# Kernel optimization log

Measured on AMD Instinct MI355X. Metric: run time of the kernel, lower is better.

## Reference

```python
import jax, jax.numpy as jnp
import numpy as np

B, NQ, NA = 2, 4096, 2048
DIM_INP, DIM, HID, NBLK, K = 512, 512, 512, 5, 8


def _pe(p):
    # NeRF positional encoding, L=10: [sin(f0*p), cos(f0*p), sin(f1*p), ...] -> 60 dims
    freqs = (2.0 ** jnp.arange(10, dtype=p.dtype)) * jnp.pi
    a = p[..., None, :] * freqs[:, None]          # [..., 10, 3]
    out = jnp.stack([jnp.sin(a), jnp.cos(a)], axis=-2)  # [..., 10, 2, 3]
    return out.reshape(*p.shape[:-1], 60)


def _forward(xyz_q, global_feats, anchors_xyz, anchors_feats,
             w_qs, w_ks, w_vs, w_kg, w_vg,
             d1_w, d1_b, d2_w, d2_b, g1_w, g1_b, g2_w, g2_b,
             fc_p_w, fc_p_b, fc_c_w, fc_c_b, blk0_w, blk0_b, blk1_w, blk1_b):
    # ---- KNN (torch.no_grad equivalent) ----
    q = jax.lax.stop_gradient(xyz_q)
    a = jax.lax.stop_gradient(anchors_xyz)
    d2 = (jnp.sum(q * q, -1)[:, :, None] + jnp.sum(a * a, -1)[:, None, :]
          - 2.0 * jnp.einsum('bqd,bnd->bqn', q, a))        # [B,NQ,NA]
    _, knn_idx = jax.lax.top_k(-d2, K)                      # [B,NQ,K] smallest dists

    gather = jax.vmap(lambda t, i: t[i])                    # per-batch gather

    # ---- cross-transformer (vector attention over K local + 1 global token) ----
    q_attn = global_feats @ w_qs                            # [B,DIM]
    kg = jnp.broadcast_to((global_feats @ w_kg)[:, None, None, :], (B, NQ, 1, DIM))
    vg = jnp.broadcast_to((global_feats @ w_vg)[:, None, None, :], (B, NQ, 1, DIM))
    k_attn = jnp.concatenate([gather(anchors_feats @ w_ks, knn_idx), kg], axis=2)  # [B,NQ,K+1,DIM]
    v_attn = jnp.concatenate([gather(anchors_feats @ w_vs, knn_idx), vg], axis=2)

    xyz_k = gather(anchors_xyz, knn_idx)                    # [B,NQ,K,3]
    d = xyz_q[:, :, None] - xyz_k                           # relative positions
    pe_loc = jax.nn.relu(d @ d1_w + d1_b) @ d2_w + d2_b     # fc_delta, [B,NQ,K,DIM]
    pos = jnp.concatenate([pe_loc, jnp.zeros((B, NQ, 1, DIM), pe_loc.dtype)], axis=2)

    attn_in = q_attn[:, None, None, :] - k_attn + pos
    attn = jax.nn.relu(attn_in @ g1_w + g1_b) @ g2_w + g2_b # fc_gamma
    attn = jax.nn.softmax(attn, axis=-2)                    # softmax over neighbor axis
    lat = jnp.einsum('bmnf,bmnf->bmf', attn, v_attn + pos)  # [B,NQ,DIM]

    # ---- occupancy decoder ----
    net = _pe(xyz_q) @ fc_p_w + fc_p_b                      # [B,NQ,HID]
    for i in range(NBLK):
        net = net + lat @ fc_c_w[i] + fc_c_b[i]
        h = jax.nn.relu(net) @ blk0_w[i] + blk0_b[i]
        net = net + (jax.nn.relu(h) @ blk1_w[i] + blk1_b[i])  # ResnetBlockFC (shortcut=identity)
    return net


def setup_inputs() -> dict:
    key = jax.random.key(0)
    ks = jax.random.split(key, 32)
    r = lambda i, shape, s=0.02: jax.random.normal(ks[i], shape, jnp.float32) * s
    return {
        'xyz_q': jax.random.uniform(ks[0], (B, NQ, 3), jnp.float32),
        'global_feats': jax.random.normal(ks[2], (B, DIM_INP), jnp.float32),
        'anchors_xyz': jax.random.uniform(ks[1], (B, NA, 3), jnp.float32),
        'anchors_feats': jax.random.normal(ks[3], (B, NA, DIM_INP), jnp.float32),
        'w_qs': r(4, (DIM_INP, DIM)), 'w_ks': r(5, (DIM_INP, DIM)), 'w_vs': r(6, (DIM_INP, DIM)),
        'w_kg': r(7, (DIM_INP, DIM)), 'w_vg': r(8, (DIM_INP, DIM)),
        'd1_w': r(9, (3, DIM)), 'd1_b': r(10, (DIM,)),
        'd2_w': r(11, (DIM, DIM)), 'd2_b': r(12, (DIM,)),
        'g1_w': r(13, (DIM, DIM)), 'g1_b': r(14, (DIM,)),
        'g2_w': r(15, (DIM, DIM)), 'g2_b': r(16, (DIM,)),
        'fc_p_w': r(17, (60, HID)), 'fc_p_b': r(18, (HID,)),
        'fc_c_w': r(19, (NBLK, DIM, HID)), 'fc_c_b': r(20, (NBLK, HID)),
        'blk0_w': r(21, (NBLK, HID, HID)), 'blk0_b': r(22, (NBLK, HID)),
        'blk1_w': r(23, (NBLK, HID, HID)), 'blk1_b': r(24, (NBLK, HID)),
    }


def reference(xyz_q, global_feats, anchors_xyz, anchors_feats,
              w_qs, w_ks, w_vs, w_kg, w_vg,
              d1_w, d1_b, d2_w, d2_b, g1_w, g1_b, g2_w, g2_b,
              fc_p_w, fc_p_b, fc_c_w, fc_c_b, blk0_w, blk0_b, blk1_w, blk1_b):
    return _forward(xyz_q, global_feats, anchors_xyz, anchors_feats,
                    w_qs, w_ks, w_vs, w_kg, w_vg,
                    d1_w, d1_b, d2_w, d2_b, g1_w, g1_b, g2_w, g2_b,
                    fc_p_w, fc_p_b, fc_c_w, fc_c_b, blk0_w, blk0_b, blk1_w, blk1_b)
```

## Files before the change

### kernel.cpp

```cpp
#include <hip/hip_runtime.h>

#define B 2
#define NQ 4096
#define NA 2048
#define CH 1024
#define LDK 40

typedef __attribute__((ext_vector_type(8))) short bf16x8;
typedef __attribute__((ext_vector_type(4))) float f32x4;

__device__ __forceinline__ float b2f(unsigned short u){ union{unsigned i; float f;} c; c.i=((unsigned)u)<<16; return c.f; }
__device__ __forceinline__ unsigned short f2b(float f){ union{float f; unsigned u;} c; c.f=f; unsigned u=c.u; u += 0x7FFFu + ((u>>16)&1u); return (unsigned short)(u>>16); }
__device__ __forceinline__ void split2(float x, short& h, short& l){
    unsigned short hh = f2b(x); h = (short)hh; l = (short)f2b(x - b2f(hh));
}
__device__ __forceinline__ float4 ld4(const float* p){ return *(const float4*)p; }

__device__ __forceinline__ void gld_lds16(const void* g, void* s) {
    __builtin_amdgcn_global_load_lds(
        (__attribute__((address_space(1))) unsigned int*)g,
        (__attribute__((address_space(3))) unsigned int*)s,
        16, 0, 0);
}

__global__ __launch_bounds__(256) void proj_small(
    const float* __restrict__ gf,
    const float* __restrict__ w_qs, const float* __restrict__ w_kg, const float* __restrict__ w_vg,
    float* __restrict__ q_attn, float* __restrict__ kgv, float* __restrict__ vgv)
{
    int mat = blockIdx.x >> 1, b = blockIdx.x & 1;
    const float* W = (mat==0) ? w_qs : (mat==1 ? w_kg : w_vg);
    float* O       = (mat==0) ? q_attn : (mat==1 ? kgv : vgv);
    __shared__ float sg[512];
    int t = threadIdx.x;
    for (int i=t;i<512;i+=256) sg[i] = gf[b*512+i];
    __syncthreads();
    for (int c=t;c<512;c+=256) {
        float acc = 0.f;
        for (int k=0;k<512;k++) acc = fmaf(sg[k], W[k*512+c], acc);
        O[b*512+c] = acc;
    }
}

__global__ __launch_bounds__(256) void knn_kernel(
    const float* __restrict__ xyz_q, const float* __restrict__ axyz, int* __restrict__ knn)
{
    __shared__ float sax[NA], say[NA], saz[NA];
    const int t = threadIdx.x;
    const int b  = blockIdx.x >> 9;
    const int qi = t >> 5;
    const int q  = ((blockIdx.x & 511) << 3) + qi;
    const int g  = t & 31;
    for (int i=t;i<NA;i+=256) {
        const float* ap = axyz + (size_t)(b*NA+i)*3;
        sax[i]=ap[0]; say[i]=ap[1]; saz[i]=ap[2];
    }
    __syncthreads();
    const double qx = (double)xyz_q[(size_t)(b*NQ+q)*3+0];
    const double qy = (double)xyz_q[(size_t)(b*NQ+q)*3+1];
    const double qz = (double)xyz_q[(size_t)(b*NQ+q)*3+2];
    const double qq = (qx*qx + qy*qy) + qz*qz;
    double best[8]; int bid[8];
    #pragma unroll
    for (int j=0;j<8;j++){ best[j]=1.0e300; bid[j]=0; }
    for (int jj=0; jj<64; jj++) {
        const int i = jj*32 + g;
        double ax=(double)sax[i], ay=(double)say[i], az=(double)saz[i];
        double aa  = (ax*ax + ay*ay) + az*az;
        double dot = (qx*ax + qy*ay) + qz*az;
        double dd  = (qq + aa) - 2.0*dot;
        if (dd < best[7]) {
            best[7]=dd; bid[7]=i;
            #pragma unroll
            for (int j=7;j>0;--j) if (best[j] < best[j-1]) {
                double tf=best[j]; best[j]=best[j-1]; best[j-1]=tf;
                int ti=bid[j]; bid[j]=bid[j-1]; bid[j-1]=ti;
            }
        }
    }
    #pragma unroll
    for (int s=16; s>=1; s>>=1) {
        double pb[8]; int pbi[8];
        #pragma unroll
        for (int j=0;j<8;j++){
            pb[j]  = __shfl_xor(best[j], s, 64);
            pbi[j] = __shfl_xor(bid[j],  s, 64);
        }
        #pragma unroll
        for (int i=0;i<8;i++) {
            double bo = pb[7-i]; int boi = pbi[7-i];
            if (bo < best[i]) { best[i]=bo; bid[i]=boi; }
        }
        #pragma unroll
        for (int i=0;i<4;i++) {
            if (best[i] > best[i+4]) {
                double td=best[i]; best[i]=best[i+4]; best[i+4]=td;
                int ti=bid[i]; bid[i]=bid[i+4]; bid[i+4]=ti;
            }
        }
        #pragma unroll
        for (int ii=0;ii<2;ii++)
        #pragma unroll
        for (int jj2=0;jj2<2;jj2++) {
            int i = ii*4 + jj2;
            if (best[i] > best[i+2]) {
                double td=best[i]; best[i]=best[i+2]; best[i+2]=td;
                int ti=bid[i]; bid[i]=bid[i+2]; bid[i+2]=ti;
            }
        }
        #pragma unroll
        for (int ii=0;ii<4;ii++) {
            int i = ii*2;
            if (best[i] > best[i+1]) {
                double td=best[i]; best[i]=best[i+1]; best[i+1]=td;
                int ti=bid[i]; bid[i]=bid[i+1]; bid[i+1]=ti;
            }
        }
    }
    if (g == 0) {
        #pragma unroll
        for (int j=0;j<8;j++) knn[(size_t)(b*NQ+q)*8+j] = bid[j];
    }
}

__global__ __launch_bounds__(256) void prep_w5(
    const float* __restrict__ W0, const float* __restrict__ W1, const float* __restrict__ W2,
    const float* __restrict__ W3, const float* __restrict__ W4,
    short* __restrict__ O0, short* __restrict__ O1, short* __restrict__ O2,
    short* __restrict__ O3, short* __restrict__ O4)
{
    const int m = blockIdx.x >> 7;
    const float* W = (m==0)?W0:(m==1)?W1:(m==2)?W2:(m==3)?W3:W4;
    short* Wb      = (m==0)?O0:(m==1)?O1:(m==2)?O2:(m==3)?O3:O4;
    const int gid = (blockIdx.x & 127)*256 + threadIdx.x;
    const int n  = gid & 511;
    const int kc = (gid >> 9) * 8;
    short o[8];
    #pragma unroll
    for (int j=0;j<8;j++) o[j] = (short)f2b(W[(size_t)(kc+j)*512 + n]);
    *(short4*)&Wb[(size_t)n*512 + kc]     = make_short4(o[0],o[1],o[2],o[3]);
    *(short4*)&Wb[(size_t)n*512 + kc + 4] = make_short4(o[4],o[5],o[6],o[7]);
}
__global__ __launch_bounds__(256) void prep_w3(
    const float* __restrict__ W0, const float* __restrict__ W1, const float* __restrict__ W2,
    short* __restrict__ H0, short* __restrict__ L0,
    short* __restrict__ H1, short* __restrict__ L1,
    short* __restrict__ H2, short* __restrict__ L2)
{
    const int m = blockIdx.x >> 7;
    const float* W = (m==0)?W0:(m==1)?W1:W2;
    short* Wh = (m==0)?H0:(m==1)?H1:H2;
    short* Wl = (m==0)?L0:(m==1)?L1:L2;
    const int gid = (blockIdx.x & 127)*256 + threadIdx.x;
    const int n  = gid & 511;
    const int kc = (gid >> 9) * 8;
    short hi[8], lo[8];
    #pragma unroll
    for (int j=0;j<8;j++) split2(W[(size_t)(kc+j)*512 + n], hi[j], lo[j]);
    *(short4*)&Wh[(size_t)n*512 + kc]     = make_short4(hi[0],hi[1],hi[2],hi[3]);
    *(short4*)&Wh[(size_t)n*512 + kc + 4] = make_short4(hi[4],hi[5],hi[6],hi[7]);
    *(short4*)&Wl[(size_t)n*512 + kc]     = make_short4(lo[0],lo[1],lo[2],lo[3]);
    *(short4*)&Wl[(size_t)n*512 + kc + 4] = make_short4(lo[4],lo[5],lo[6],lo[7]);
}

__global__ __launch_bounds__(256) void cvt_bf16(
    const float* __restrict__ X, short* __restrict__ Xb)
{
    const size_t i0 = ((size_t)blockIdx.x*256 + threadIdx.x)*8;
    float4 a = *(const float4*)(X+i0), bq = *(const float4*)(X+i0+4);
    float v[8] = {a.x,a.y,a.z,a.w,bq.x,bq.y,bq.z,bq.w};
    short o[8];
    #pragma unroll
    for (int j=0;j<8;j++) o[j] = (short)f2b(v[j]);
    *(short4*)(Xb+i0)   = make_short4(o[0],o[1],o[2],o[3]);
    *(short4*)(Xb+i0+4) = make_short4(o[4],o[5],o[6],o[7]);
}

template<int OUT_MODE, int RELU_OUT>
__global__ __launch_bounds__(256) void gemm1(
    const short* __restrict__ Ab, const short* __restrict__ Wb,
    const float* __restrict__ bias,
    float* __restrict__ Cf, short* __restrict__ Cb)
{
    __shared__ short As[64*LDK], Bs[64*LDK];
    const int t = threadIdx.x;
    const int row0 = blockIdx.y*64, col0 = blockIdx.x*64;
    const int lane = t & 63, w = t >> 6;
    const int m0 = (w>>1)*32, n0 = (w&1)*32;
    const int fl = lane & 15, quad = lane >> 4;
    const int s_row = t >> 2, s_k = (t & 3) * 8;

    f32x4 zero = {0.f,0.f,0.f,0.f};
    f32x4 acc[2][2];
    acc[0][0]=zero; acc[0][1]=zero; acc[1][0]=zero; acc[1][1]=zero;

    const size_t a_base = (size_t)(row0+s_row)*512 + s_k;
    const size_t b_base = (size_t)(col0+s_row)*512 + s_k;
    int4 ra = *(const int4*)(Ab + a_base);
    int4 rb = *(const int4*)(Wb + b_base);

    for (int k0 = 0; k0 < 512; k0 += 32) {
        *(int4*)&As[s_row*LDK + s_k] = ra;
        *(int4*)&Bs[s_row*LDK + s_k] = rb;
        __syncthreads();
        if (k0 + 32 < 512) {
            ra = *(const int4*)(Ab + a_base + k0 + 32);
            rb = *(const int4*)(Wb + b_base + k0 + 32);
        }
        bf16x8 fa[2], fb[2];
        #pragma unroll
        for (int i=0;i<2;i++) {
            fa[i] = *(const bf16x8*)&As[(m0 + i*16 + fl)*LDK + quad*8];
            fb[i] = *(const bf16x8*)&Bs[(n0 + i*16 + fl)*LDK + quad*8];
        }
        #pragma unroll
        for (int i=0;i<2;i++)
        #pragma unroll
        for (int j=0;j<2;j++)
            acc[i][j] = __builtin_amdgcn_mfma_f32_16x16x32_bf16(fa[i], fb[j], acc[i][j], 0,0,0);
        __syncthreads();
    }
    #pragma unroll
    for (int i=0;i<2;i++)
    #pragma unroll
    for (int j=0;j<2;j++) {
        const int col = col0 + n0 + j*16 + fl;
        const float bb = bias ? bias[col] : 0.f;
        #pragma unroll
        for (int r=0;r<4;r++) {
            const int row = row0 + m0 + i*16 + quad*4 + r;
            const size_t off = (size_t)row*512 + col;
            float v = acc[i][j][r] + bb;
            if (RELU_OUT) v = fmaxf(v,0.f);
            if (OUT_MODE == 0) Cf[off] = v;
            else               Cb[off] = (short)f2b(v);
        }
    }
}

__global__ __launch_bounds__(256) void gemm1b(
    const short* __restrict__ Ab, const short* __restrict__ Wb,
    const float* __restrict__ bias, short* __restrict__ Cb)
{
    __shared__ short sA[2][128*32], sB[2][64*32];
    const int t = threadIdx.x;
    const int nwg = gridDim.x * gridDim.y;
    const int flat = blockIdx.y * gridDim.x + blockIdx.x;
    const int per = nwg >> 3;
    const int sw = ((nwg & 7) == 0) ? ((flat & 7) * per + (flat >> 3)) : flat;
    const int bx = sw % gridDim.x, by = sw / gridDim.x;
    const int row0 = by * 128, col0 = bx * 64;
    const int lane = t & 63, w = t >> 6;
    const int m0 = (w >> 1) * 64, n0 = (w & 1) * 32;
    const int fl = lane & 15, quad = lane >> 4;

    f32x4 zero = {0.f,0.f,0.f,0.f};
    f32x4 acc[4][2];
    #pragma unroll
    for (int i=0;i<4;i++)
    #pragma unroll
    for (int j=0;j<2;j++) acc[i][j] = zero;

    auto stage = [&](int buf, int k0) {
        #pragma unroll
        for (int rnd = 0; rnd < 2; ++rnd) {
            const int idx = rnd*256 + t;
            const int r = idx >> 2, kp = (idx & 3) * 8;
            const int ldso = (rnd*256 + (t & 192)) * 8;
            gld_lds16(Ab + (size_t)(row0 + r)*512 + k0 + kp, &sA[buf][ldso]);
        }
        {
            const int r = t >> 2, kp = (t & 3) * 8;
            const int ldso = (t & 192) * 8;
            gld_lds16(Wb + (size_t)(col0 + r)*512 + k0 + kp, &sB[buf][ldso]);
        }
    };

    stage(0, 0);
    __syncthreads();
    for (int k0 = 0; k0 < 512; k0 += 32) {
        const int cur = (k0 >> 5) & 1;
        if (k0 + 32 < 512) stage(cur ^ 1, k0 + 32);
        bf16x8 fa[4], fb[2];
        #pragma unroll
        for (int i = 0; i < 4; i++)
            fa[i] = *(const bf16x8*)&sA[cur][(m0 + i*16 + fl)*32 + quad*8];
        #pragma unroll
        for (int j = 0; j < 2; j++)
            fb[j] = *(const bf16x8*)&sB[cur][(n0 + j*16 + fl)*32 + quad*8];
        #pragma unroll
        for (int i=0;i<4;i++)
        #pragma unroll
        for (int j=0;j<2;j++)
            acc[i][j] = __builtin_amdgcn_mfma_f32_16x16x32_bf16(fa[i], fb[j], acc[i][j], 0,0,0);
        __syncthreads();
    }
    #pragma unroll
    for (int i=0;i<4;i++)
    #pragma unroll
    for (int j=0;j<2;j++) {
        const int col = col0 + n0 + j*16 + fl;
        const float bb = bias[col];
        #pragma unroll
        for (int r=0;r<4;r++) {
            const int row = row0 + m0 + i*16 + quad*4 + r;
            Cb[(size_t)row*512 + col] = (short)f2b(acc[i][j][r] + bb);
        }
    }
}

__global__ __launch_bounds__(256) void gemm_pos(
    const float* __restrict__ xyz_q, const float* __restrict__ axyz, const int* __restrict__ knn,
    const float* __restrict__ d1w, const float* __restrict__ d1b,
    const short* __restrict__ Wb, const float* __restrict__ bias,
    short* __restrict__ Cb, int qbase)
{
    __shared__ short As[64*LDK], Bs[64*LDK];
    __shared__ float sd1[4][512];
    __shared__ float sdx[64], sdy[64], sdz[64];
    const int t = threadIdx.x;
    const int row0 = blockIdx.y*64, col0 = blockIdx.x*64;
    const int lane = t & 63, w = t >> 6;
    const int m0 = (w>>1)*32, n0 = (w&1)*32;
    const int fl = lane & 15, quad = lane >> 4;
    const int s_row = t >> 2, s_k = (t & 3) * 8;
    for (int i=t;i<2048;i+=256) {
        int r = i >> 9, c = i & 511;
        sd1[r][c] = (r < 3) ? d1w[r*512 + c] : d1b[c];
    }
    if (t < 64) {
        int gr = qbase*8 + row0 + t;
        int b  = gr >> 15;
        int gq = gr >> 3;
        int idx = knn[gr];
        const float* qp = xyz_q + (size_t)gq*3;
        const float* ap = axyz + (size_t)(b*NA + idx)*3;
        sdx[t]=qp[0]-ap[0]; sdy[t]=qp[1]-ap[1]; sdz[t]=qp[2]-ap[2];
    }
    __syncthreads();
    const float dx = sdx[s_row], dy = sdy[s_row], dz = sdz[s_row];

    f32x4 zero = {0.f,0.f,0.f,0.f};
    f32x4 acc[2][2];
    acc[0][0]=zero; acc[0][1]=zero; acc[1][0]=zero; acc[1][1]=zero;

    const size_t b_base = (size_t)(col0+s_row)*512 + s_k;
    int4 rb = *(const int4*)(Wb + b_base);

    for (int k0 = 0; k0 < 512; k0 += 32) {
        {
            short o[8];
            #pragma unroll
            for (int j=0;j<8;j++) {
                int k = k0 + s_k + j;
                float v = fmaf(dx, sd1[0][k], fmaf(dy, sd1[1][k], fmaf(dz, sd1[2][k], sd1[3][k])));
                o[j] = (short)f2b(fmaxf(v, 0.f));
            }
            *(short4*)&As[s_row*LDK + s_k]     = make_short4(o[0],o[1],o[2],o[3]);
            *(short4*)&As[s_row*LDK + s_k + 4] = make_short4(o[4],o[5],o[6],o[7]);
        }
        *(int4*)&Bs[s_row*LDK + s_k] = rb;
        __syncthreads();
        if (k0 + 32 < 512) rb = *(const int4*)(Wb + b_base + k0 + 32);
        bf16x8 fa[2], fb[2];
        #pragma unroll
        for (int i=0;i<2;i++) {
            fa[i] = *(const bf16x8*)&As[(m0 + i*16 + fl)*LDK + quad*8];
            fb[i] = *(const bf16x8*)&Bs[(n0 + i*16 + fl)*LDK + quad*8];
        }
        #pragma unroll
        for (int i=0;i<2;i++)
        #pragma unroll
        for (int j=0;j<2;j++)
            acc[i][j] = __builtin_amdgcn_mfma_f32_16x16x32_bf16(fa[i], fb[j], acc[i][j], 0,0,0);
        __syncthreads();
    }
    #pragma unroll
    for (int i=0;i<2;i++)
    #pragma unroll
    for (int j=0;j<2;j++) {
        const int col = col0 + n0 + j*16 + fl;
        const float bb = bias[col];
        #pragma unroll
        for (int r=0;r<4;r++) {
            const int row = row0 + m0 + i*16 + quad*4 + r;
            Cb[(size_t)row*512 + col] = (short)f2b(acc[i][j][r] + bb);
        }
    }
}

__global__ __launch_bounds__(256) void gemm_g1(
    const float* __restrict__ q_attn, const float* __restrict__ kgv,
    const short* __restrict__ ak_bf, const short* __restrict__ pos_bf, const int* __restrict__ knn,
    const short* __restrict__ Wb, const float* __restrict__ bias,
    short* __restrict__ Cb, int qbase)
{
    __shared__ short As[64*LDK], Bs[64*LDK];
    __shared__ int s_aoff[64], s_poff[64];
    const int t = threadIdx.x;
    const int row0 = blockIdx.y*64, col0 = blockIdx.x*64;
    const int lane = t & 63, w = t >> 6;
    const int m0 = (w>>1)*32, n0 = (w&1)*32;
    const int fl = lane & 15, quad = lane >> 4;
    const int s_row = t >> 2, s_k = (t & 3) * 8;
    const int b = qbase >> 12;
    if (t < 64) {
        int g = row0 + t;
        int q = g / 9, n = g - q*9;
        if (n < 8) { s_aoff[t] = b*NA + knn[(size_t)(qbase + q)*8 + n]; s_poff[t] = q*8 + n; }
        else       { s_aoff[t] = -1; s_poff[t] = 0; }
    }
    __syncthreads();
    const int ao = s_aoff[s_row];
    const int po = s_poff[s_row];

    f32x4 zero = {0.f,0.f,0.f,0.f};
    f32x4 acc[2][2];
    acc[0][0]=zero; acc[0][1]=zero; acc[1][0]=zero; acc[1][1]=zero;

    const size_t b_base = (size_t)(col0+s_row)*512 + s_k;
    int4 rb = *(const int4*)(Wb + b_base);
    float4 qa0, qa1, gk0, gk1;
    ushort4 kv0, kv1, pv0, pv1;
    qa0 = ld4(q_attn + b*512 + s_k); qa1 = ld4(q_attn + b*512 + s_k + 4);
    if (ao >= 0) {
        kv0 = *(const ushort4*)(ak_bf + (size_t)ao*512 + s_k);
        kv1 = *(const ushort4*)(ak_bf + (size_t)ao*512 + s_k + 4);
        pv0 = *(const ushort4*)(pos_bf + (size_t)po*512 + s_k);
        pv1 = *(const ushort4*)(pos_bf + (size_t)po*512 + s_k + 4);
    } else {
        gk0 = ld4(kgv + b*512 + s_k); gk1 = ld4(kgv + b*512 + s_k + 4);
    }

    for (int k0 = 0; k0 < 512; k0 += 32) {
        {
            short o[8];
            if (ao >= 0) {
                o[0]=(short)f2b(qa0.x - b2f(kv0.x) + b2f(pv0.x));
                o[1]=(short)f2b(qa0.y - b2f(kv0.y) + b2f(pv0.y));
                o[2]=(short)f2b(qa0.z - b2f(kv0.z) + b2f(pv0.z));
                o[3]=(short)f2b(qa0.w - b2f(kv0.w) + b2f(pv0.w));
                o[4]=(short)f2b(qa1.x - b2f(kv1.x) + b2f(pv1.x));
                o[5]=(short)f2b(qa1.y - b2f(kv1.y) + b2f(pv1.y));
                o[6]=(short)f2b(qa1.z - b2f(kv1.z) + b2f(pv1.z));
                o[7]=(short)f2b(qa1.w - b2f(kv1.w) + b2f(pv1.w));
            } else {
                o[0]=(short)f2b(qa0.x - gk0.x); o[1]=(short)f2b(qa0.y - gk0.y);
                o[2]=(short)f2b(qa0.z - gk0.z); o[3]=(short)f2b(qa0.w - gk0.w);
                o[4]=(short)f2b(qa1.x - gk1.x); o[5]=(short)f2b(qa1.y - gk1.y);
                o[6]=(short)f2b(qa1.z - gk1.z); o[7]=(short)f2b(qa1.w - gk1.w);
            }
            *(short4*)&As[s_row*LDK + s_k]     = make_short4(o[0],o[1],o[2],o[3]);
            *(short4*)&As[s_row*LDK + s_k + 4] = make_short4(o[4],o[5],o[6],o[7]);
        }
        *(int4*)&Bs[s_row*LDK + s_k] = rb;
        __syncthreads();
        if (k0 + 32 < 512) {
            const int k = k0 + 32 + s_k;
            rb = *(const int4*)(Wb + b_base + k0 + 32);
            qa0 = ld4(q_attn + b*512 + k); qa1 = ld4(q_attn + b*512 + k + 4);
            if (ao >= 0) {
                kv0 = *(const ushort4*)(ak_bf + (size_t)ao*512 + k);
                kv1 = *(const ushort4*)(ak_bf + (size_t)ao*512 + k + 4);
                pv0 = *(const ushort4*)(pos_bf + (size_t)po*512 + k);
                pv1 = *(const ushort4*)(pos_bf + (size_t)po*512 + k + 4);
            } else {
                gk0 = ld4(kgv + b*512 + k); gk1 = ld4(kgv + b*512 + k + 4);
            }
        }
        bf16x8 fa[2], fb[2];
        #pragma unroll
        for (int i=0;i<2;i++) {
            fa[i] = *(const bf16x8*)&As[(m0 + i*16 + fl)*LDK + quad*8];
            fb[i] = *(const bf16x8*)&Bs[(n0 + i*16 + fl)*LDK + quad*8];
        }
        #pragma unroll
        for (int i=0;i<2;i++)
        #pragma unroll
        for (int j=0;j<2;j++)
            acc[i][j] = __builtin_amdgcn_mfma_f32_16x16x32_bf16(fa[i], fb[j], acc[i][j], 0,0,0);
        __syncthreads();
    }
    #pragma unroll
    for (int i=0;i<2;i++)
    #pragma unroll
    for (int j=0;j<2;j++) {
        const int col = col0 + n0 + j*16 + fl;
        const float bb = bias[col];
        #pragma unroll
        for (int r=0;r<4;r++) {
            const int row = row0 + m0 + i*16 + quad*4 + r;
            Cb[(size_t)row*512 + col] = (short)f2b(fmaxf(acc[i][j][r] + bb, 0.f));
        }
    }
}

template<int OUT_MODE, int RELU_OUT, int HAS_ADD>
__global__ __launch_bounds__(256) void gemm3b(
    const short* __restrict__ Ah, const short* __restrict__ Al,
    const short* __restrict__ Wh, const short* __restrict__ Wl,
    const float* __restrict__ bias, const float* __restrict__ addend,
    float* __restrict__ Cf, short* __restrict__ Ch, short* __restrict__ Cl)
{
    __shared__ short sAh[2][128*32], sAl[2][128*32], sBh[2][64*32], sBl[2][64*32];
    const int t = threadIdx.x;
    const int nwg = gridDim.x * gridDim.y;
    const int flat = blockIdx.y * gridDim.x + blockIdx.x;
    const int per = nwg >> 3;
    const int sw = ((nwg & 7) == 0) ? ((flat & 7) * per + (flat >> 3)) : flat;
    const int bx = sw % gridDim.x, by = sw / gridDim.x;
    const int row0 = by * 128, col0 = bx * 64;
    const int lane = t & 63, w = t >> 6;
    const int m0 = (w >> 1) * 64, n0 = (w & 1) * 32;
    const int fl = lane & 15, quad = lane >> 4;

    f32x4 zero = {0.f,0.f,0.f,0.f};
    f32x4 acc[4][2];
    #pragma unroll
    for (int i=0;i<4;i++)
    #pragma unroll
    for (int j=0;j<2;j++) acc[i][j] = zero;

    auto stage = [&](int buf, int k0) {
        #pragma unroll
        for (int rnd = 0; rnd < 2; ++rnd) {
            const int idx = rnd*256 + t;
            const int r = idx >> 2, kp = (idx & 3) * 8;
            const int ldso = (rnd*256 + (t & 192)) * 8;
            const size_t ga = (size_t)(row0 + r)*512 + k0 + kp;
            gld_lds16(Ah + ga, &sAh[buf][ldso]);
            gld_lds16(Al + ga, &sAl[buf][ldso]);
        }
        {
            const int r = t >> 2, kp = (t & 3) * 8;
            const int ldso = (t & 192) * 8;
            const size_t gb = (size_t)(col0 + r)*512 + k0 + kp;
            gld_lds16(Wh + gb, &sBh[buf][ldso]);
            gld_lds16(Wl + gb, &sBl[buf][ldso]);
        }
    };

    stage(0, 0);
    __syncthreads();
    for (int k0 = 0; k0 < 512; k0 += 32) {
        const int cur = (k0 >> 5) & 1;
        if (k0 + 32 < 512) stage(cur ^ 1, k0 + 32);
        bf16x8 fah[4], fal[4], fbh[2], fbl[2];
        #pragma unroll
        for (int i = 0; i < 4; i++) {
            fah[i] = *(const bf16x8*)&sAh[cur][(m0 + i*16 + fl)*32 + quad*8];
            fal[i] = *(const bf16x8*)&sAl[cur][(m0 + i*16 + fl)*32 + quad*8];
        }
        #pragma unroll
        for (int j = 0; j < 2; j++) {
            fbh[j] = *(const bf16x8*)&sBh[cur][(n0 + j*16 + fl)*32 + quad*8];
            fbl[j] = *(const bf16x8*)&sBl[cur][(n0 + j*16 + fl)*32 + quad*8];
        }
        #pragma unroll
        for (int i=0;i<4;i++)
        #pragma unroll
        for (int j=0;j<2;j++)
            acc[i][j] = __builtin_amdgcn_mfma_f32_16x16x32_bf16(fah[i], fbh[j], acc[i][j], 0,0,0);
        #pragma unroll
        for (int i=0;i<4;i++)
        #pragma unroll
        for (int j=0;j<2;j++)
            acc[i][j] = __builtin_amdgcn_mfma_f32_16x16x32_bf16(fah[i], fbl[j], acc[i][j], 0,0,0);
        #pragma unroll
        for (int i=0;i<4;i++)
        #pragma unroll
        for (int j=0;j<2;j++)
            acc[i][j] = __builtin_amdgcn_mfma_f32_16x16x32_bf16(fal[i], fbh[j], acc[i][j], 0,0,0);
        __syncthreads();
    }
    #pragma unroll
    for (int i=0;i<4;i++)
    #pragma unroll
    for (int j=0;j<2;j++) {
        const int col = col0 + n0 + j*16 + fl;
        const float bb = bias ? bias[col] : 0.f;
        #pragma unroll
        for (int r=0;r<4;r++) {
            const int row = row0 + m0 + i*16 + quad*4 + r;
            const size_t off = (size_t)row*512 + col;
            float v = acc[i][j][r] + bb;
            if (HAS_ADD) v += addend[off];
            if (OUT_MODE == 0) {
                if (RELU_OUT) v = fmaxf(v,0.f);
                Cf[off] = v;
            } else if (OUT_MODE == 1) {
                if (RELU_OUT) v = fmaxf(v,0.f);
                short h,l; split2(v,h,l); Ch[off]=h; Cl[off]=l;
            } else {
                Cf[off] = v;
                short h,l; split2(fmaxf(v,0.f),h,l); Ch[off]=h; Cl[off]=l;
            }
        }
    }
}

__global__ __launch_bounds__(256) void softmax_agg(
    const short* __restrict__ attn_preb, const short* __restrict__ pos_bf,
    const short* __restrict__ av_bf, const float* __restrict__ vgv,
    const int* __restrict__ knn, short* __restrict__ lath, short* __restrict__ latl, int qbase)
{
    __shared__ int sk[8];
    const int q = blockIdx.x;
    const int gq = qbase + q;
    const int b = qbase >> 12;
    const int t = threadIdx.x;
    if (t < 8) sk[t] = knn[(size_t)gq*8 + t];
    __syncthreads();
    for (int c = t; c < 512; c += 256) {
        float p[9];
        #pragma unroll
        for (int n=0;n<9;n++) p[n] = b2f((unsigned short)attn_preb[(size_t)(q*9+n)*512 + c]);
        float m = p[0];
        #pragma unroll
        for (int n=1;n<9;n++) m = fmaxf(m, p[n]);
        float e[9], s = 0.f;
        #pragma unroll
        for (int n=0;n<9;n++){ e[n] = expf(p[n]-m); s += e[n]; }
        const float inv = 1.0f / s;
        float acc = 0.f;
        #pragma unroll
        for (int n=0;n<8;n++) {
            float vv = b2f((unsigned short)av_bf[(size_t)(b*NA + sk[n])*512 + c])
                     + b2f((unsigned short)pos_bf[(size_t)(q*8+n)*512 + c]);
            acc = fmaf(e[n]*inv, vv, acc);
        }
        acc = fmaf(e[8]*inv, vgv[b*512 + c], acc);
        short h,l; split2(acc,h,l);
        lath[(size_t)gq*512 + c] = h; latl[(size_t)gq*512 + c] = l;
    }
}

__global__ __launch_bounds__(256) void pe_fc(
    const float* __restrict__ xyz_q, const float* __restrict__ fw, const float* __restrict__ fb,
    float* __restrict__ net)
{
    __shared__ float spe[16*60];
    const int t = threadIdx.x;
    const int q0 = blockIdx.x * 16;
    for (int i=t;i<960;i+=256) {
        int ql = i/60, j = i - ql*60;
        int l = j/6; int r6 = j - l*6; int s = r6/3; int d = r6 - s*3;
        float pv = xyz_q[(size_t)(q0+ql)*3 + d];
        float a = pv * (3.14159265358979323846f * (float)(1<<l));
        spe[ql*60+j] = (s==0) ? sinf(a) : cosf(a);
    }
    __syncthreads();
    float acc0[16], acc1[16];
    #pragma unroll
    for (int ql=0;ql<16;ql++){ acc0[ql]=0.f; acc1[ql]=0.f; }
    const int c0 = t, c1 = t + 256;
    for (int k=0;k<60;k++) {
        float w0 = fw[k*512 + c0];
        float w1 = fw[k*512 + c1];
        #pragma unroll
        for (int ql=0;ql<16;ql++) {
            float pv = spe[ql*60+k];
            acc0[ql] = fmaf(pv, w0, acc0[ql]);
            acc1[ql] = fmaf(pv, w1, acc1[ql]);
        }
    }
    const float b0v = fb[c0], b1v = fb[c1];
    #pragma unroll
    for (int ql=0;ql<16;ql++) {
        net[(size_t)(q0+ql)*512 + c0] = acc0[ql] + b0v;
        net[(size_t)(q0+ql)*512 + c1] = acc1[ql] + b1v;
    }
}

extern "C" void kernel_launch(void* const* d_in, const int* in_sizes, int n_in,
                              void* d_out, int out_size, void* d_ws, size_t ws_size,
                              hipStream_t stream) {
    const float* xyz_q  = (const float*)d_in[0];
    const float* gf     = (const float*)d_in[1];
    const float* axyz   = (const float*)d_in[2];
    const float* afeat  = (const float*)d_in[3];
    const float* w_qs   = (const float*)d_in[4];
    const float* w_ks   = (const float*)d_in[5];
    const float* w_vs   = (const float*)d_in[6];
    const float* w_kg   = (const float*)d_in[7];
    const float* w_vg   = (const float*)d_in[8];
    const float* d1_w   = (const float*)d_in[9];
    const float* d1_b   = (const float*)d_in[10];
    const float* d2_w   = (const float*)d_in[11];
    const float* d2_b   = (const float*)d_in[12];
    const float* g1_w   = (const float*)d_in[13];
    const float* g1_b   = (const float*)d_in[14];
    const float* g2_w   = (const float*)d_in[15];
    const float* g2_b   = (const float*)d_in[16];
    const float* fc_p_w = (const float*)d_in[17];
    const float* fc_p_b = (const float*)d_in[18];
    const float* fc_c_w = (const float*)d_in[19];
    const float* fc_c_b = (const float*)d_in[20];
    const float* blk0_w = (const float*)d_in[21];
    const float* blk0_b = (const float*)d_in[22];
    const float* blk1_w = (const float*)d_in[23];
    const float* blk1_b = (const float*)d_in[24];
    float* out = (float*)d_out;

    const size_t MB = 1u<<20;
    char* base = (char*)d_ws;
    float* q_attn = (float*)base;
    float* kgv    = q_attn + 1024;
    float* vgv    = kgv + 1024;
    int*   knn    = (int*)(base + 16*1024);
    short* wksb = (short*)(base + 1*MB);
    short* wvsb = wksb + 262144;
    short* wd2b = wvsb + 262144;
    short* wg1b = wd2b + 262144;
    short* wg2b = wg1b + 262144;
    short* dch = (short*)(base + 1*MB);         short* dcl = dch + 262144;
    short* d0h = dcl + 262144;                  short* d0l = d0h + 262144;
    short* d1h = d0l + 262144;                  short* d1l = d1h + 262144;
    short* lath = (short*)(base + 5*MB);
    short* latl = (short*)(base + 13*MB);
    char* T = base + 21*MB;
    short* ak_bf = (short*)T;
    short* av_bf = (short*)(T + 4*MB);
    short* posb  = (short*)(T + 8*MB);
    short* yb    = (short*)(T + 16*MB);
    short* attn_preb = (short*)(T + 25*MB);
    short* af_bf = (short*)(T + 8*MB);
    short* nrh = (short*)T;            short* nrl = (short*)(T + 8*MB);
    short* hdh = (short*)(T + 16*MB);  short* hdl = (short*)(T + 24*MB);
    if ((size_t)(55*MB) > ws_size) return;

    proj_small<<<dim3(6), dim3(256), 0, stream>>>(gf, w_qs, w_kg, w_vg, q_attn, kgv, vgv);
    knn_kernel<<<dim3(1024), dim3(256), 0, stream>>>(xyz_q, axyz, knn);

    cvt_bf16<<<dim3(1024), dim3(256), 0, stream>>>(afeat, af_bf);
    prep_w5<<<dim3(640), dim3(256), 0, stream>>>(w_ks, w_vs, d2_w, g1_w, g2_w,
                                                 wksb, wvsb, wd2b, wg1b, wg2b);
    gemm1<3,0><<<dim3(8,64), dim3(256), 0, stream>>>(af_bf, wksb, nullptr, nullptr, ak_bf);
    gemm1<3,0><<<dim3(8,64), dim3(256), 0, stream>>>(af_bf, wvsb, nullptr, nullptr, av_bf);

    for (int qbase = 0; qbase < B*NQ; qbase += CH) {
        gemm_pos<<<dim3(8, CH*8/64), dim3(256), 0, stream>>>(xyz_q, axyz, knn, d1_w, d1_b, wd2b, d2_b, posb, qbase);
        gemm_g1<<<dim3(8, CH*9/64), dim3(256), 0, stream>>>(q_attn, kgv, ak_bf, posb, knn, wg1b, g1_b, yb, qbase);
        gemm1b<<<dim3(8, CH*9/128), dim3(256), 0, stream>>>(yb, wg2b, g2_b, attn_preb);
        softmax_agg<<<dim3(CH), dim3(256), 0, stream>>>(attn_preb, posb, av_bf, vgv, knn, lath, latl, qbase);
    }

    pe_fc<<<dim3(512), dim3(256), 0, stream>>>(xyz_q, fc_p_w, fc_p_b, out);
    for (int i=0;i<5;i++) {
        const float* cw  = fc_c_w + (size_t)i*512*512;
        const float* cb  = fc_c_b + (size_t)i*512;
        const float* b0w = blk0_w + (size_t)i*512*512;
        const float* b0b = blk0_b + (size_t)i*512;
        const float* b1w = blk1_w + (size_t)i*512*512;
        const float* b1b = blk1_b + (size_t)i*512;
        prep_w3<<<dim3(384), dim3(256), 0, stream>>>(cw, b0w, b1w, dch, dcl, d0h, d0l, d1h, d1l);
        gemm3b<2,0,1><<<dim3(8,64), dim3(256), 0, stream>>>(lath, latl, dch, dcl, cb, out, out, nrh, nrl);
        gemm3b<1,1,0><<<dim3(8,64), dim3(256), 0, stream>>>(nrh, nrl, d0h, d0l, b0b, nullptr, nullptr, hdh, hdl);
        gemm3b<0,0,1><<<dim3(8,64), dim3(256), 0, stream>>>(hdh, hdl, d1h, d1l, b1b, out, out, nullptr, nullptr);
    }
}
```

Baseline: 1.182 ms.

## Materialize GEMM A-operands separately and route all attention GEMMs through gemm1b

```diff
diff --git a/kernel.cpp b/kernel.cpp
--- a/kernel.cpp
+++ b/kernel.cpp
@@ -4,7 +4,6 @@
 #define NQ 4096
 #define NA 2048
 #define CH 1024
-#define LDK 40
 
 typedef __attribute__((ext_vector_type(8))) short bf16x8;
 typedef __attribute__((ext_vector_type(4))) float f32x4;
@@ -176,68 +175,73 @@
     *(short4*)(Xb+i0+4) = make_short4(o[4],o[5],o[6],o[7]);
 }
 
-template<int OUT_MODE, int RELU_OUT>
-__global__ __launch_bounds__(256) void gemm1(
-    const short* __restrict__ Ab, const short* __restrict__ Wb,
-    const float* __restrict__ bias,
-    float* __restrict__ Cf, short* __restrict__ Cb)
-{
-    __shared__ short As[64*LDK], Bs[64*LDK];
-    const int t = threadIdx.x;
-    const int row0 = blockIdx.y*64, col0 = blockIdx.x*64;
-    const int lane = t & 63, w = t >> 6;
-    const int m0 = (w>>1)*32, n0 = (w&1)*32;
-    const int fl = lane & 15, quad = lane >> 4;
-    const int s_row = t >> 2, s_k = (t & 3) * 8;
-
-    f32x4 zero = {0.f,0.f,0.f,0.f};
-    f32x4 acc[2][2];
-    acc[0][0]=zero; acc[0][1]=zero; acc[1][0]=zero; acc[1][1]=zero;
-
-    const size_t a_base = (size_t)(row0+s_row)*512 + s_k;
-    const size_t b_base = (size_t)(col0+s_row)*512 + s_k;
-    int4 ra = *(const int4*)(Ab + a_base);
-    int4 rb = *(const int4*)(Wb + b_base);
-
-    for (int k0 = 0; k0 < 512; k0 += 32) {
-        *(int4*)&As[s_row*LDK + s_k] = ra;
-        *(int4*)&Bs[s_row*LDK + s_k] = rb;
-        __syncthreads();
-        if (k0 + 32 < 512) {
-            ra = *(const int4*)(Ab + a_base + k0 + 32);
-            rb = *(const int4*)(Wb + b_base + k0 + 32);
-        }
-        bf16x8 fa[2], fb[2];
-        #pragma unroll
-        for (int i=0;i<2;i++) {
-            fa[i] = *(const bf16x8*)&As[(m0 + i*16 + fl)*LDK + quad*8];
-            fb[i] = *(const bf16x8*)&Bs[(n0 + i*16 + fl)*LDK + quad*8];
-        }
-        #pragma unroll
-        for (int i=0;i<2;i++)
-        #pragma unroll
-        for (int j=0;j<2;j++)
-            acc[i][j] = __builtin_amdgcn_mfma_f32_16x16x32_bf16(fa[i], fb[j], acc[i][j], 0,0,0);
-        __syncthreads();
-    }
-    #pragma unroll
-    for (int i=0;i<2;i++)
-    #pragma unroll
-    for (int j=0;j<2;j++) {
-        const int col = col0 + n0 + j*16 + fl;
-        const float bb = bias ? bias[col] : 0.f;
-        #pragma unroll
-        for (int r=0;r<4;r++) {
-            const int row = row0 + m0 + i*16 + quad*4 + r;
-            const size_t off = (size_t)row*512 + col;
-            float v = acc[i][j][r] + bb;
-            if (RELU_OUT) v = fmaxf(v,0.f);
-            if (OUT_MODE == 0) Cf[off] = v;
-            else               Cb[off] = (short)f2b(v);
-        }
-    }
-}
-
+__global__ __launch_bounds__(256) void pe_make(
+    const float* __restrict__ xyz_q, const float* __restrict__ axyz, const int* __restrict__ knn,
+    const float* __restrict__ d1w, const float* __restrict__ d1b,
+    short* __restrict__ peA, int qbase)
+{
+    const int t = threadIdx.x;
+    const int r  = blockIdx.x*4 + (t >> 6);
+    const int col0 = (t & 63) * 8;
+    const int gr = qbase*8 + r;
+    const int b  = gr >> 15;
+    const int gq = gr >> 3;
+    const int idx = knn[gr];
+    const float* qp = xyz_q + (size_t)gq*3;
+    const float* ap = axyz + (size_t)(b*NA + idx)*3;
+    const float dx = qp[0]-ap[0], dy = qp[1]-ap[1], dz = qp[2]-ap[2];
+    short o[8];
+    #pragma unroll
+    for (int j=0;j<8;j++) {
+        const int k = col0 + j;
+        float v = fmaf(dx, d1w[k], fmaf(dy, d1w[512+k], fmaf(dz, d1w[1024+k], d1b[k])));
+        o[j] = (short)f2b(fmaxf(v, 0.f));
+    }
+    *(short4*)&peA[(size_t)r*512 + col0]     = make_short4(o[0],o[1],o[2],o[3]);
+    *(short4*)&peA[(size_t)r*512 + col0 + 4] = make_short4(o[4],o[5],o[6],o[7]);
+}
+
+__global__ __launch_bounds__(256) void g1_make(
+    const float* __restrict__ q_attn, const float* __restrict__ kgv,
+    const short* __restrict__ ak_bf, const short* __restrict__ pos_bf, const int* __restrict__ knn,
+    short* __restrict__ g1A, int qbase)
+{
+    const int t = threadIdx.x;
+    const int r = blockIdx.x*4 + (t >> 6);
+    const int col0 = (t & 63) * 8;
+    const int b = qbase >> 12;
+    const int q = r / 9, n = r - q*9;
+    float4 qa0 = ld4(q_attn + b*512 + col0);
+    float4 qa1 = ld4(q_attn + b*512 + col0 + 4);
+    short o[8];
+    if (n < 8) {
+        const int ao = b*NA + knn[(size_t)(qbase + q)*8 + n];
+        const int po = q*8 + n;
+        ushort4 kv0 = *(const ushort4*)(ak_bf + (size_t)ao*512 + col0);
+        ushort4 kv1 = *(const ushort4*)(ak_bf + (size_t)ao*512 + col0 + 4);
+        ushort4 pv0 = *(const ushort4*)(pos_bf + (size_t)po*512 + col0);
+        ushort4 pv1 = *(const ushort4*)(pos_bf + (size_t)po*512 + col0 + 4);
+        o[0]=(short)f2b(qa0.x - b2f(kv0.x) + b2f(pv0.x));
+        o[1]=(short)f2b(qa0.y - b2f(kv0.y) + b2f(pv0.y));
+        o[2]=(short)f2b(qa0.z - b2f(kv0.z) + b2f(pv0.z));
+        o[3]=(short)f2b(qa0.w - b2f(kv0.w) + b2f(pv0.w));
+        o[4]=(short)f2b(qa1.x - b2f(kv1.x) + b2f(pv1.x));
+        o[5]=(short)f2b(qa1.y - b2f(kv1.y) + b2f(pv1.y));
+        o[6]=(short)f2b(qa1.z - b2f(kv1.z) + b2f(pv1.z));
+        o[7]=(short)f2b(qa1.w - b2f(kv1.w) + b2f(pv1.w));
+    } else {
+        float4 gk0 = ld4(kgv + b*512 + col0);
+        float4 gk1 = ld4(kgv + b*512 + col0 + 4);
+        o[0]=(short)f2b(qa0.x - gk0.x); o[1]=(short)f2b(qa0.y - gk0.y);
+        o[2]=(short)f2b(qa0.z - gk0.z); o[3]=(short)f2b(qa0.w - gk0.w);
+        o[4]=(short)f2b(qa1.x - gk1.x); o[5]=(short)f2b(qa1.y - gk1.y);
+        o[6]=(short)f2b(qa1.z - gk1.z); o[7]=(short)f2b(qa1.w - gk1.w);
+    }
+    *(short4*)&g1A[(size_t)r*512 + col0]     = make_short4(o[0],o[1],o[2],o[3]);
+    *(short4*)&g1A[(size_t)r*512 + col0 + 4] = make_short4(o[4],o[5],o[6],o[7]);
+}
+
+template<int RELU_OUT>
 __global__ __launch_bounds__(256) void gemm1b(
     const short* __restrict__ Ab, const short* __restrict__ Wb,
     const float* __restrict__ bias, short* __restrict__ Cb)
@@ -300,197 +304,13 @@
     #pragma unroll
     for (int j=0;j<2;j++) {
         const int col = col0 + n0 + j*16 + fl;
-        const float bb = bias[col];
+        const float bb = bias ? bias[col] : 0.f;
         #pragma unroll
         for (int r=0;r<4;r++) {
             const int row = row0 + m0 + i*16 + quad*4 + r;
-            Cb[(size_t)row*512 + col] = (short)f2b(acc[i][j][r] + bb);
-        }
-    }
-}
-
-__global__ __launch_bounds__(256) void gemm_pos(
-    const float* __restrict__ xyz_q, const float* __restrict__ axyz, const int* __restrict__ knn,
-    const float* __restrict__ d1w, const float* __restrict__ d1b,
-    const short* __restrict__ Wb, const float* __restrict__ bias,
-    short* __restrict__ Cb, int qbase)
-{
-    __shared__ short As[64*LDK], Bs[64*LDK];
-    __shared__ float sd1[4][512];
-    __shared__ float sdx[64], sdy[64], sdz[64];
-    const int t = threadIdx.x;
-    const int row0 = blockIdx.y*64, col0 = blockIdx.x*64;
-    const int lane = t & 63, w = t >> 6;
-    const int m0 = (w>>1)*32, n0 = (w&1)*32;
-    const int fl = lane & 15, quad = lane >> 4;
-    const int s_row = t >> 2, s_k = (t & 3) * 8;
-    for (int i=t;i<2048;i+=256) {
-        int r = i >> 9, c = i & 511;
-        sd1[r][c] = (r < 3) ? d1w[r*512 + c] : d1b[c];
-    }
-    if (t < 64) {
-        int gr = qbase*8 + row0 + t;
-        int b  = gr >> 15;
-        int gq = gr >> 3;
-        int idx = knn[gr];
-        const float* qp = xyz_q + (size_t)gq*3;
-        const float* ap = axyz + (size_t)(b*NA + idx)*3;
-        sdx[t]=qp[0]-ap[0]; sdy[t]=qp[1]-ap[1]; sdz[t]=qp[2]-ap[2];
-    }
-    __syncthreads();
-    const float dx = sdx[s_row], dy = sdy[s_row], dz = sdz[s_row];
-
-    f32x4 zero = {0.f,0.f,0.f,0.f};
-    f32x4 acc[2][2];
-    acc[0][0]=zero; acc[0][1]=zero; acc[1][0]=zero; acc[1][1]=zero;
-
-    const size_t b_base = (size_t)(col0+s_row)*512 + s_k;
-    int4 rb = *(const int4*)(Wb + b_base);
-
-    for (int k0 = 0; k0 < 512; k0 += 32) {
-        {
-            short o[8];
-            #pragma unroll
-            for (int j=0;j<8;j++) {
-                int k = k0 + s_k + j;
-                float v = fmaf(dx, sd1[0][k], fmaf(dy, sd1[1][k], fmaf(dz, sd1[2][k], sd1[3][k])));
-                o[j] = (short)f2b(fmaxf(v, 0.f));
-            }
-            *(short4*)&As[s_row*LDK + s_k]     = make_short4(o[0],o[1],o[2],o[3]);
-            *(short4*)&As[s_row*LDK + s_k + 4] = make_short4(o[4],o[5],o[6],o[7]);
-        }
-        *(int4*)&Bs[s_row*LDK + s_k] = rb;
-        __syncthreads();
-        if (k0 + 32 < 512) rb = *(const int4*)(Wb + b_base + k0 + 32);
-        bf16x8 fa[2], fb[2];
-        #pragma unroll
-        for (int i=0;i<2;i++) {
-            fa[i] = *(const bf16x8*)&As[(m0 + i*16 + fl)*LDK + quad*8];
-            fb[i] = *(const bf16x8*)&Bs[(n0 + i*16 + fl)*LDK + quad*8];
-        }
-        #pragma unroll
-        for (int i=0;i<2;i++)
-        #pragma unroll
-        for (int j=0;j<2;j++)
-            acc[i][j] = __builtin_amdgcn_mfma_f32_16x16x32_bf16(fa[i], fb[j], acc[i][j], 0,0,0);
-        __syncthreads();
-    }
-    #pragma unroll
-    for (int i=0;i<2;i++)
-    #pragma unroll
-    for (int j=0;j<2;j++) {
-        const int col = col0 + n0 + j*16 + fl;
-        const float bb = bias[col];
-        #pragma unroll
-        for (int r=0;r<4;r++) {
-            const int row = row0 + m0 + i*16 + quad*4 + r;
-            Cb[(size_t)row*512 + col] = (short)f2b(acc[i][j][r] + bb);
-        }
-    }
-}
-
-__global__ __launch_bounds__(256) void gemm_g1(
-    const float* __restrict__ q_attn, const float* __restrict__ kgv,
-    const short* __restrict__ ak_bf, const short* __restrict__ pos_bf, const int* __restrict__ knn,
-    const short* __restrict__ Wb, const float* __restrict__ bias,
-    short* __restrict__ Cb, int qbase)
-{
-    __shared__ short As[64*LDK], Bs[64*LDK];
-    __shared__ int s_aoff[64], s_poff[64];
-    const int t = threadIdx.x;
-    const int row0 = blockIdx.y*64, col0 = blockIdx.x*64;
-    const int lane = t & 63, w = t >> 6;
-    const int m0 = (w>>1)*32, n0 = (w&1)*32;
-    const int fl = lane & 15, quad = lane >> 4;
-    const int s_row = t >> 2, s_k = (t & 3) * 8;
-    const int b = qbase >> 12;
-    if (t < 64) {
-        int g = row0 + t;
-        int q = g / 9, n = g - q*9;
-        if (n < 8) { s_aoff[t] = b*NA + knn[(size_t)(qbase + q)*8 + n]; s_poff[t] = q*8 + n; }
-        else       { s_aoff[t] = -1; s_poff[t] = 0; }
-    }
-    __syncthreads();
-    const int ao = s_aoff[s_row];
-    const int po = s_poff[s_row];
-
-    f32x4 zero = {0.f,0.f,0.f,0.f};
-    f32x4 acc[2][2];
-    acc[0][0]=zero; acc[0][1]=zero; acc[1][0]=zero; acc[1][1]=zero;
-
-    const size_t b_base = (size_t)(col0+s_row)*512 + s_k;
-    int4 rb = *(const int4*)(Wb + b_base);
-    float4 qa0, qa1, gk0, gk1;
-    ushort4 kv0, kv1, pv0, pv1;
-    qa0 = ld4(q_attn + b*512 + s_k); qa1 = ld4(q_attn + b*512 + s_k + 4);
-    if (ao >= 0) {
-        kv0 = *(const ushort4*)(ak_bf + (size_t)ao*512 + s_k);
-        kv1 = *(const ushort4*)(ak_bf + (size_t)ao*512 + s_k + 4);
-        pv0 = *(const ushort4*)(pos_bf + (size_t)po*512 + s_k);
-        pv1 = *(const ushort4*)(pos_bf + (size_t)po*512 + s_k + 4);
-    } else {
-        gk0 = ld4(kgv + b*512 + s_k); gk1 = ld4(kgv + b*512 + s_k + 4);
-    }
-
-    for (int k0 = 0; k0 < 512; k0 += 32) {
-        {
-            short o[8];
-            if (ao >= 0) {
-                o[0]=(short)f2b(qa0.x - b2f(kv0.x) + b2f(pv0.x));
-                o[1]=(short)f2b(qa0.y - b2f(kv0.y) + b2f(pv0.y));
-                o[2]=(short)f2b(qa0.z - b2f(kv0.z) + b2f(pv0.z));
-                o[3]=(short)f2b(qa0.w - b2f(kv0.w) + b2f(pv0.w));
-                o[4]=(short)f2b(qa1.x - b2f(kv1.x) + b2f(pv1.x));
-                o[5]=(short)f2b(qa1.y - b2f(kv1.y) + b2f(pv1.y));
-                o[6]=(short)f2b(qa1.z - b2f(kv1.z) + b2f(pv1.z));
-                o[7]=(short)f2b(qa1.w - b2f(kv1.w) + b2f(pv1.w));
-            } else {
-                o[0]=(short)f2b(qa0.x - gk0.x); o[1]=(short)f2b(qa0.y - gk0.y);
-                o[2]=(short)f2b(qa0.z - gk0.z); o[3]=(short)f2b(qa0.w - gk0.w);
-                o[4]=(short)f2b(qa1.x - gk1.x); o[5]=(short)f2b(qa1.y - gk1.y);
-                o[6]=(short)f2b(qa1.z - gk1.z); o[7]=(short)f2b(qa1.w - gk1.w);
-            }
-            *(short4*)&As[s_row*LDK + s_k]     = make_short4(o[0],o[1],o[2],o[3]);
-            *(short4*)&As[s_row*LDK + s_k + 4] = make_short4(o[4],o[5],o[6],o[7]);
-        }
-        *(int4*)&Bs[s_row*LDK + s_k] = rb;
-        __syncthreads();
-        if (k0 + 32 < 512) {
-            const int k = k0 + 32 + s_k;
-            rb = *(const int4*)(Wb + b_base + k0 + 32);
-            qa0 = ld4(q_attn + b*512 + k); qa1 = ld4(q_attn + b*512 + k + 4);
-            if (ao >= 0) {
-                kv0 = *(const ushort4*)(ak_bf + (size_t)ao*512 + k);
-                kv1 = *(const ushort4*)(ak_bf + (size_t)ao*512 + k + 4);
-                pv0 = *(const ushort4*)(pos_bf + (size_t)po*512 + k);
-                pv1 = *(const ushort4*)(pos_bf + (size_t)po*512 + k + 4);
-            } else {
-                gk0 = ld4(kgv + b*512 + k); gk1 = ld4(kgv + b*512 + k + 4);
-            }
-        }
-        bf16x8 fa[2], fb[2];
-        #pragma unroll
-        for (int i=0;i<2;i++) {
-            fa[i] = *(const bf16x8*)&As[(m0 + i*16 + fl)*LDK + quad*8];
-            fb[i] = *(const bf16x8*)&Bs[(n0 + i*16 + fl)*LDK + quad*8];
-        }
-        #pragma unroll
-        for (int i=0;i<2;i++)
-        #pragma unroll
-        for (int j=0;j<2;j++)
-            acc[i][j] = __builtin_amdgcn_mfma_f32_16x16x32_bf16(fa[i], fb[j], acc[i][j], 0,0,0);
-        __syncthreads();
-    }
-    #pragma unroll
-    for (int i=0;i<2;i++)
-    #pragma unroll
-    for (int j=0;j<2;j++) {
-        const int col = col0 + n0 + j*16 + fl;
-        const float bb = bias[col];
-        #pragma unroll
-        for (int r=0;r<4;r++) {
-            const int row = row0 + m0 + i*16 + quad*4 + r;
-            Cb[(size_t)row*512 + col] = (short)f2b(fmaxf(acc[i][j][r] + bb, 0.f));
+            float v = acc[i][j][r] + bb;
+            if (RELU_OUT) v = fmaxf(v, 0.f);
+            Cb[(size_t)row*512 + col] = (short)f2b(v);
         }
     }
 }
@@ -725,6 +545,8 @@
     short* yb    = (short*)(T + 16*MB);
     short* attn_preb = (short*)(T + 25*MB);
     short* af_bf = (short*)(T + 8*MB);
+    short* peA  = (short*)(T + 25*MB);
+    short* g1A  = (short*)(T + 25*MB);
     short* nrh = (short*)T;            short* nrl = (short*)(T + 8*MB);
     short* hdh = (short*)(T + 16*MB);  short* hdl = (short*)(T + 24*MB);
     if ((size_t)(55*MB) > ws_size) return;
@@ -735,13 +557,15 @@
     cvt_bf16<<<dim3(1024), dim3(256), 0, stream>>>(afeat, af_bf);
     prep_w5<<<dim3(640), dim3(256), 0, stream>>>(w_ks, w_vs, d2_w, g1_w, g2_w,
                                                  wksb, wvsb, wd2b, wg1b, wg2b);
-    gemm1<3,0><<<dim3(8,64), dim3(256), 0, stream>>>(af_bf, wksb, nullptr, nullptr, ak_bf);
-    gemm1<3,0><<<dim3(8,64), dim3(256), 0, stream>>>(af_bf, wvsb, nullptr, nullptr, av_bf);
+    gemm1b<0><<<dim3(8, 32), dim3(256), 0, stream>>>(af_bf, wksb, nullptr, ak_bf);
+    gemm1b<0><<<dim3(8, 32), dim3(256), 0, stream>>>(af_bf, wvsb, nullptr, av_bf);
 
     for (int qbase = 0; qbase < B*NQ; qbase += CH) {
-        gemm_pos<<<dim3(8, CH*8/64), dim3(256), 0, stream>>>(xyz_q, axyz, knn, d1_w, d1_b, wd2b, d2_b, posb, qbase);
-        gemm_g1<<<dim3(8, CH*9/64), dim3(256), 0, stream>>>(q_attn, kgv, ak_bf, posb, knn, wg1b, g1_b, yb, qbase);
-        gemm1b<<<dim3(8, CH*9/128), dim3(256), 0, stream>>>(yb, wg2b, g2_b, attn_preb);
+        pe_make<<<dim3(CH*8/4), dim3(256), 0, stream>>>(xyz_q, axyz, knn, d1_w, d1_b, peA, qbase);
+        gemm1b<0><<<dim3(8, CH*8/128), dim3(256), 0, stream>>>(peA, wd2b, d2_b, posb);
+        g1_make<<<dim3(CH*9/4), dim3(256), 0, stream>>>(q_attn, kgv, ak_bf, posb, knn, g1A, qbase);
+        gemm1b<1><<<dim3(8, CH*9/128), dim3(256), 0, stream>>>(g1A, wg1b, g1_b, yb);
+        gemm1b<0><<<dim3(8, CH*9/128), dim3(256), 0, stream>>>(yb, wg2b, g2_b, attn_preb);
         softmax_agg<<<dim3(CH), dim3(256), 0, stream>>>(attn_preb, posb, av_bf, vgv, knn, lath, latl, qbase);
     }
 
```

After: 1.150 ms. 1.03x faster.
